# Kernel optimization log

Measured on AMD Instinct MI355X. Metric: run time of the kernel, lower is better.

The kernel has to match this reference:

```python
import jax, jax.numpy as jnp
import numpy as np

H = 8
D = 64
EPS = 1e-5
TEMP = 1.0


def _ln(x, w, b):
    m = jnp.mean(x, axis=-1, keepdims=True)
    v = jnp.var(x, axis=-1, keepdims=True)
    return (x - m) * jax.lax.rsqrt(v + EPS) * w + b


def setup_inputs() -> dict:
    key = jax.random.key(0)
    ks = jax.random.split(key, 8)
    B, T, C = 4, 1024, 512
    x = jax.random.normal(ks[0], (B, T, C), dtype=jnp.float32)
    pair = jax.random.normal(ks[1], (B, T, T, H), dtype=jnp.float32)
    mask = jax.random.randint(ks[2], (B, T, T), 0, 2).astype(bool)
    s = 0.02
    return {
        "x": x,
        "pair": pair,
        "mask": mask,
        "norm_w": jnp.ones((C,), jnp.float32),
        "norm_b": jnp.zeros((C,), jnp.float32),
        "qkv_w": jax.random.normal(ks[3], (3 * C, C), jnp.float32) * s,
        "qkv_b": jnp.zeros((3 * C,), jnp.float32),
        "qln_w": jnp.ones((C,), jnp.float32),
        "qln_b": jnp.zeros((C,), jnp.float32),
        "kln_w": jnp.ones((C,), jnp.float32),
        "kln_b": jnp.zeros((C,), jnp.float32),
        "proj_w": jax.random.normal(ks[4], (C, C), jnp.float32) * s,
        "proj_b": jnp.zeros((C,), jnp.float32),
    }


def reference(x, pair, mask, norm_w, norm_b, qkv_w, qkv_b, qln_w, qln_b,
              kln_w, kln_b, proj_w, proj_b):
    B, T, C = x.shape
    # pre-norm
    xn = _ln(x, norm_w, norm_b)
    qkv = xn @ qkv_w.T + qkv_b  # [B,T,3C]
    q, k, v = jnp.split(qkv, 3, axis=-1)
    q = _ln(q, qln_w, qln_b)
    k = _ln(k, kln_w, kln_b)
    # [B,T,C] -> [B,H,T,D]
    to_heads = lambda t: t.reshape(B, T, H, D).transpose(0, 2, 1, 3)
    q, k, v = to_heads(q), to_heads(k), to_heads(v)
    scale = (D ** -0.5) / TEMP
    sim = jnp.einsum("bhid,bhjd->bhij", q, k) * scale
    sim = sim + pair.transpose(0, 3, 1, 2)  # additive pair bias [B,H,T,T]
    neg = jnp.finfo(sim.dtype).min
    sim = jnp.where(mask[:, None, :, :], sim, sim + neg)
    attn = jax.nn.softmax(sim, axis=-1)
    out = jnp.einsum("bhij,bhjd->bhid", attn, v)
    out = out.transpose(0, 2, 1, 3).reshape(B, T, C)
    return out @ proj_w.T + proj_b
```

## Files before the change

### kernel.cpp

```cpp
#include <hip/hip_runtime.h>
#include <math.h>

#define B_  4
#define T_  1024
#define C_  512
#define H_  8
#define D_  64
#define N3_ 1536
#define BT_ 4096

constexpr float kEps = 1e-5f;
constexpr float kNeg = -3.4028234663852886e38f;
constexpr float kMaskNeg = -1e38f;
constexpr float kShift = 12.0f;

typedef __attribute__((ext_vector_type(8))) short bf16x8;
typedef __attribute__((ext_vector_type(4))) float f32x4;

__device__ __forceinline__ short f2bf(float f) {
  union { float f; unsigned u; } v; v.f = f;
  unsigned r = v.u + 0x7FFFu + ((v.u >> 16) & 1u);
  return (short)(r >> 16);
}
__device__ __forceinline__ float bf2f(unsigned short b) {
  union { unsigned u; float f; } v;
  v.u = ((unsigned)b) << 16;
  return v.f;
}

__device__ __forceinline__ void gld16(const void* g, void* l) {
  __builtin_amdgcn_global_load_lds(
      (const __attribute__((address_space(1))) unsigned int*)g,
      (__attribute__((address_space(3))) unsigned int*)l, 16, 0, 0);
}

__global__ __launch_bounds__(64) void mask_detect_kernel(
    const unsigned int* __restrict__ m, int* __restrict__ flag) {
  int lane = threadIdx.x;
  int any_big = 0;
#pragma unroll
  for (int p = 0; p < 16; ++p) {
    unsigned int v = m[lane + p * 64];
    any_big |= (v > 1u);
  }
  unsigned long long b = __ballot(any_big);
  if (lane == 0) flag[0] = (b != 0ull) ? 1 : 0;
}

__global__ __launch_bounds__(256) void mask_convert_kernel(
    const void* __restrict__ mraw, const int* __restrict__ flag,
    uchar4* __restrict__ out) {
  int idx = blockIdx.x * 256 + threadIdx.x;
  uchar4 v;
  if (flag[0]) {
    v = ((const uchar4*)mraw)[idx];
    v.x = v.x ? 1 : 0; v.y = v.y ? 1 : 0; v.z = v.z ? 1 : 0; v.w = v.w ? 1 : 0;
  } else {
    int4 w = ((const int4*)mraw)[idx];
    v = make_uchar4(w.x != 0, w.y != 0, w.z != 0, w.w != 0);
  }
  out[idx] = v;
}

__global__ __launch_bounds__(256) void pair_prep_kernel(
    const float* __restrict__ pair, const void* __restrict__ mraw,
    short* __restrict__ biast) {
  __shared__ short P[8][1024 + 8];
  unsigned wv = ((const unsigned*)mraw)[threadIdx.x];
  int is_u8 = __syncthreads_or(wv > 1u);
  int bi = blockIdx.x;
  int b = bi >> 10, i = bi & 1023;
  int tid = threadIdx.x;
  const float* src = pair + (size_t)bi * (T_ * H_);
#pragma unroll
  for (int p = 0; p < 8; ++p) {
    int c = tid + p * 256;
    int j = c >> 1, hh = (c & 1) * 4;
    float4 v = *(const float4*)&src[c * 4];
    P[hh + 0][j] = f2bf(v.x);
    P[hh + 1][j] = f2bf(v.y);
    P[hh + 2][j] = f2bf(v.z);
    P[hh + 3][j] = f2bf(v.w);
  }
  bool mk[4];
  if (is_u8) {
    uchar4 mv = ((const uchar4*)mraw)[bi * 256 + tid];
    mk[0] = mv.x; mk[1] = mv.y; mk[2] = mv.z; mk[3] = mv.w;
  } else {
    int4 mv = ((const int4*)mraw)[bi * 256 + tid];
    mk[0] = mv.x != 0; mk[1] = mv.y != 0; mk[2] = mv.z != 0; mk[3] = mv.w != 0;
  }
  __syncthreads();
  const short negb = f2bf(kMaskNeg);
  int j = tid * 4;
#pragma unroll
  for (int h = 0; h < 8; ++h) {
    short4 o;
    o.x = mk[0] ? P[h][j + 0] : negb;
    o.y = mk[1] ? P[h][j + 1] : negb;
    o.z = mk[2] ? P[h][j + 2] : negb;
    o.w = mk[3] ? P[h][j + 3] : negb;
    *(short4*)&biast[((size_t)(b * 8 + h) * T_ + i) * T_ + j] = o;
  }
}

__global__ __launch_bounds__(256) void wcvt2_kernel(
    const float* __restrict__ a, short* __restrict__ oa,
    const float* __restrict__ b, short* __restrict__ ob, int nblk_a) {
  int bid = blockIdx.x;
  const float* src; short* dst; int idx;
  if (bid < nblk_a) { src = a; dst = oa; idx = bid * 256 + threadIdx.x; }
  else             { src = b; dst = ob; idx = (bid - nblk_a) * 256 + threadIdx.x; }
  int i = idx * 4;
  float4 v = *(const float4*)&src[i];
  short4 o;
  o.x = f2bf(v.x); o.y = f2bf(v.y); o.z = f2bf(v.z); o.w = f2bf(v.w);
  *(short4*)&dst[i] = o;
}

__global__ __launch_bounds__(128) void ln_x_kernel(
    const float* __restrict__ x, const float* __restrict__ w,
    const float* __restrict__ b, short* __restrict__ xn) {
  int row = blockIdx.x;
  int tid = threadIdx.x;
  const float* xr = x + (size_t)row * C_;
  float4 v = *(const float4*)&xr[tid * 4];
  float s  = v.x + v.y + v.z + v.w;
  float ss = v.x * v.x + v.y * v.y + v.z * v.z + v.w * v.w;
#pragma unroll
  for (int o = 32; o > 0; o >>= 1) {
    s  += __shfl_down(s, o);
    ss += __shfl_down(ss, o);
  }
  __shared__ float sh[4];
  int wid = tid >> 6, lane = tid & 63;
  if (lane == 0) { sh[wid] = s; sh[2 + wid] = ss; }
  __syncthreads();
  float m   = (sh[0] + sh[1]) * (1.0f / C_);
  float var = (sh[2] + sh[3]) * (1.0f / C_) - m * m;
  float inv = rsqrtf(var + kEps);
  float4 wv = *(const float4*)&w[tid * 4];
  float4 bv = *(const float4*)&b[tid * 4];
  short4 o4;
  o4.x = f2bf((v.x - m) * inv * wv.x + bv.x);
  o4.y = f2bf((v.y - m) * inv * wv.y + bv.y);
  o4.z = f2bf((v.z - m) * inv * wv.z + bv.z);
  o4.w = f2bf((v.w - m) * inv * wv.w + bv.w);
  *(short4*)&xn[(size_t)row * C_ + tid * 4] = o4;
}

__global__ __launch_bounds__(256) void gemm_bf16_kernel(
    const short* __restrict__ A, const short* __restrict__ W,
    const float* __restrict__ bias, float* __restrict__ Cmat,
    int M, int N, int K) {
  __shared__ short As[128 * 64];
  __shared__ short Bs[64 * 64];
  int tid = threadIdx.x;
  int lane = tid & 63, wave = tid >> 6;
  int wm = wave >> 1, wn = wave & 1;
  int col = lane & 15, quad = lane >> 4;
  int m0 = blockIdx.y * 128, n0 = blockIdx.x * 64;
  int wbase = tid & ~63;

  f32x4 acc[4][2];
#pragma unroll
  for (int mi = 0; mi < 4; ++mi)
#pragma unroll
    for (int ni = 0; ni < 2; ++ni) acc[mi][ni] = {0.f, 0.f, 0.f, 0.f};

  for (int k0 = 0; k0 < K; k0 += 64) {
    __syncthreads();
#pragma unroll
    for (int p = 0; p < 4; ++p) {
      int c = tid + p * 256;
      int row = c >> 3, kc = (c & 7) * 8;
      gld16(&A[(size_t)(m0 + row) * K + k0 + kc],
            &As[(wbase + p * 256) * 8]);
    }
#pragma unroll
    for (int p = 0; p < 2; ++p) {
      int c = tid + p * 256;
      int row = c >> 3, kc = (c & 7) * 8;
      gld16(&W[(size_t)(n0 + row) * K + k0 + kc],
            &Bs[(wbase + p * 256) * 8]);
    }
    __syncthreads();
#pragma unroll
    for (int s = 0; s < 2; ++s) {
      bf16x8 af[4], bf[2];
#pragma unroll
      for (int mi = 0; mi < 4; ++mi)
        af[mi] = *(const bf16x8*)&As[(64 * wm + 16 * mi + col) * 64 + s * 32 + quad * 8];
#pragma unroll
      for (int ni = 0; ni < 2; ++ni)
        bf[ni] = *(const bf16x8*)&Bs[(32 * wn + 16 * ni + col) * 64 + s * 32 + quad * 8];
#pragma unroll
      for (int mi = 0; mi < 4; ++mi)
#pragma unroll
        for (int ni = 0; ni < 2; ++ni)
          acc[mi][ni] = __builtin_amdgcn_mfma_f32_16x16x32_bf16(
              af[mi], bf[ni], acc[mi][ni], 0, 0, 0);
    }
  }
#pragma unroll
  for (int ni = 0; ni < 2; ++ni) {
    int n = n0 + 32 * wn + 16 * ni + col;
    float bv = bias[n];
#pragma unroll
    for (int mi = 0; mi < 4; ++mi) {
#pragma unroll
      for (int r = 0; r < 4; ++r) {
        int m = m0 + 64 * wm + 16 * mi + quad * 4 + r;
        Cmat[(size_t)m * N + n] = acc[mi][ni][r] + bv;
      }
    }
  }
}

__global__ __launch_bounds__(128) void qkv_ln_split_kernel(
    const float* __restrict__ qkv,
    const float* __restrict__ qw, const float* __restrict__ qb,
    const float* __restrict__ kw, const float* __restrict__ kb,
    short* __restrict__ qh, short* __restrict__ kh, short* __restrict__ vh) {
  int row = blockIdx.x;
  int b = row >> 10, t = row & 1023;
  int tid = threadIdx.x;
  const float* base = qkv + (size_t)row * N3_;
  int c4 = tid * 4;
  float4 qv = *(const float4*)&base[c4];
  float4 kv = *(const float4*)&base[C_ + c4];
  float4 vv = *(const float4*)&base[2 * C_ + c4];
  float sq  = qv.x + qv.y + qv.z + qv.w;
  float sqq = qv.x * qv.x + qv.y * qv.y + qv.z * qv.z + qv.w * qv.w;
  float sk  = kv.x + kv.y + kv.z + kv.w;
  float skk = kv.x * kv.x + kv.y * kv.y + kv.z * kv.z + kv.w * kv.w;
#pragma unroll
  for (int o = 32; o > 0; o >>= 1) {
    sq  += __shfl_down(sq, o);
    sqq += __shfl_down(sqq, o);
    sk  += __shfl_down(sk, o);
    skk += __shfl_down(skk, o);
  }
  __shared__ float sh[8];
  int wid = tid >> 6, lane = tid & 63;
  if (lane == 0) { sh[wid] = sq; sh[2 + wid] = sqq; sh[4 + wid] = sk; sh[6 + wid] = skk; }
  __syncthreads();
  float qm   = (sh[0] + sh[1]) * (1.0f / C_);
  float qvar = (sh[2] + sh[3]) * (1.0f / C_) - qm * qm;
  float km   = (sh[4] + sh[5]) * (1.0f / C_);
  float kvar = (sh[6] + sh[7]) * (1.0f / C_) - km * km;
  float qi = rsqrtf(qvar + kEps);
  float ki = rsqrtf(kvar + kEps);
  float4 qwv = *(const float4*)&qw[c4];
  float4 qbv = *(const float4*)&qb[c4];
  float4 kwv = *(const float4*)&kw[c4];
  float4 kbv = *(const float4*)&kb[c4];
  int h = tid >> 4;
  int d = (tid & 15) * 4;
  size_t dst = ((size_t)(b * H_ + h) * T_ + t) * D_ + d;
  short4 qo, ko, vo;
  qo.x = f2bf(((qv.x - qm) * qi * qwv.x + qbv.x) * 0.125f);
  qo.y = f2bf(((qv.y - qm) * qi * qwv.y + qbv.y) * 0.125f);
  qo.z = f2bf(((qv.z - qm) * qi * qwv.z + qbv.z) * 0.125f);
  qo.w = f2bf(((qv.w - qm) * qi * qwv.w + qbv.w) * 0.125f);
  ko.x = f2bf((kv.x - km) * ki * kwv.x + kbv.x);
  ko.y = f2bf((kv.y - km) * ki * kwv.y + kbv.y);
  ko.z = f2bf((kv.z - km) * ki * kwv.z + kbv.z);
  ko.w = f2bf((kv.w - km) * ki * kwv.w + kbv.w);
  vo.x = f2bf(vv.x); vo.y = f2bf(vv.y); vo.z = f2bf(vv.z); vo.w = f2bf(vv.w);
  *(short4*)&qh[dst] = qo;
  *(short4*)&kh[dst] = ko;
  *(short4*)&vh[dst] = vo;
}

__global__ __launch_bounds__(256) void attn_split_kernel(
    const short* __restrict__ qh, const short* __restrict__ kh,
    const short* __restrict__ vh, const short* __restrict__ biast,
    float* __restrict__ Opart, float* __restrict__ lpart) {
  __shared__ short Ks[64 * 72];
  __shared__ short Vt[64 * 72];
  __shared__ short Ps[64 * 72];
  int tid = threadIdx.x;
  int lane = tid & 63, w = tid >> 6;
  int col = lane & 15, quad = lane >> 4;
  int bh = blockIdx.y;
  int half = blockIdx.z;
  int i0 = blockIdx.x * 64;
  const short* Qg = qh + (size_t)bh * T_ * D_;
  const short* Kg = kh + (size_t)bh * T_ * D_;
  const short* Vg = vh + (size_t)bh * T_ * D_;
  const unsigned short* Bpu =
      (const unsigned short*)(biast + (size_t)bh * T_ * T_);

  bf16x8 qf[2];
#pragma unroll
  for (int s = 0; s < 2; ++s)
    qf[s] = *(const bf16x8*)&Qg[(size_t)(i0 + 16 * w + col) * D_ + s * 32 + quad * 8];

  float lsum[4];
  f32x4 oacc[4];
#pragma unroll
  for (int r = 0; r < 4; ++r) lsum[r] = 0.f;
#pragma unroll
  for (int dt = 0; dt < 4; ++dt) oacc[dt] = {0.f, 0.f, 0.f, 0.f};

  int jbase = half * (T_ / 2);
  for (int jj = 0; jj < T_ / 2; jj += 64) {
    int j0 = jbase + jj;
    __syncthreads();
#pragma unroll
    for (int p = 0; p < 2; ++p) {
      int c = tid + p * 256;
      int row = c >> 3, dc = (c & 7) * 8;
      *(int4*)&Ks[row * 72 + dc] =
          *(const int4*)&Kg[(size_t)(j0 + row) * D_ + dc];
    }
    {
      int j = tid & 63, d0 = (tid >> 6) * 16;
#pragma unroll
      for (int p = 0; p < 2; ++p) {
        short tmp[8];
        *(int4*)tmp = *(const int4*)&Vg[(size_t)(j0 + j) * D_ + d0 + p * 8];
#pragma unroll
        for (int q = 0; q < 8; ++q) Vt[(d0 + p * 8 + q) * 72 + j] = tmp[q];
      }
    }
    __syncthreads();

    unsigned short bsv[4][4];
#pragma unroll
    for (int r = 0; r < 4; ++r) {
      int gi = i0 + 16 * w + quad * 4 + r;
#pragma unroll
      for (int jt = 0; jt < 4; ++jt)
        bsv[r][jt] = Bpu[(size_t)gi * T_ + j0 + 16 * jt + col];
    }

    f32x4 sacc[4];
#pragma unroll
    for (int jt = 0; jt < 4; ++jt) sacc[jt] = {0.f, 0.f, 0.f, 0.f};
#pragma unroll
    for (int s = 0; s < 2; ++s) {
#pragma unroll
      for (int jt = 0; jt < 4; ++jt) {
        bf16x8 kf = *(const bf16x8*)&Ks[(16 * jt + col) * 72 + s * 32 + quad * 8];
        sacc[jt] = __builtin_amdgcn_mfma_f32_16x16x32_bf16(qf[s], kf, sacc[jt], 0, 0, 0);
      }
    }

#pragma unroll
    for (int r = 0; r < 4; ++r) {
      int li = 16 * w + quad * 4 + r;
#pragma unroll
      for (int jt = 0; jt < 4; ++jt) {
        float s = sacc[jt][r] + bf2f(bsv[r][jt]);
        float p = __expf(fminf(s - kShift, 60.0f));
        lsum[r] += p;
        Ps[li * 72 + 16 * jt + col] = f2bf(p);
      }
    }
    __syncthreads();

#pragma unroll
    for (int s = 0; s < 2; ++s) {
      bf16x8 pf = *(const bf16x8*)&Ps[(16 * w + col) * 72 + s * 32 + quad * 8];
#pragma unroll
      for (int dt = 0; dt < 4; ++dt) {
        bf16x8 vf = *(const bf16x8*)&Vt[(16 * dt + col) * 72 + s * 32 + quad * 8];
        oacc[dt] = __builtin_amdgcn_mfma_f32_16x16x32_bf16(pf, vf, oacc[dt], 0, 0, 0);
      }
    }
  }

#pragma unroll
  for (int r = 0; r < 4; ++r) {
    float l = lsum[r];
#pragma unroll
    for (int o = 1; o < 16; o <<= 1) l += __shfl_xor(l, o);
    int gi = i0 + 16 * w + quad * 4 + r;
    size_t orow = (size_t)half * 32768 + (size_t)bh * T_ + gi;
    if (col == 0) lpart[orow] = l;
#pragma unroll
    for (int dt = 0; dt < 4; ++dt)
      Opart[orow * 64 + 16 * dt + col] = oacc[dt][r];
  }
}

__global__ __launch_bounds__(256) void attn_merge_kernel(
    const float* __restrict__ Opart, const float* __restrict__ lpart,
    short* __restrict__ ao) {
  int g = blockIdx.x * 256 + threadIdx.x;
  int row = g >> 4, d4 = (g & 15) * 4;
  float4 o0 = *(const float4*)&Opart[(size_t)row * 64 + d4];
  float4 o1 = *(const float4*)&Opart[((size_t)32768 + row) * 64 + d4];
  float inv = 1.0f / (lpart[row] + lpart[32768 + row]);
  int bh = row >> 10, gi = row & 1023;
  int b = bh >> 3, h = bh & 7;
  short4 o;
  o.x = f2bf((o0.x + o1.x) * inv);
  o.y = f2bf((o0.y + o1.y) * inv);
  o.z = f2bf((o0.z + o1.z) * inv);
  o.w = f2bf((o0.w + o1.w) * inv);
  *(short4*)&ao[((size_t)(b * T_ + gi)) * C_ + h * D_ + d4] = o;
}

__global__ __launch_bounds__(256) void attn_kernel(
    const short* __restrict__ qh, const short* __restrict__ kh,
    const short* __restrict__ vh, const float* __restrict__ pair,
    const unsigned char* __restrict__ mask, short* __restrict__ ao) {
  __shared__ short Ks[64 * 72];
  __shared__ short Vt[64 * 72];
  __shared__ short Ps[64 * 72];
  int tid = threadIdx.x;
  int lane = tid & 63, w = tid >> 6;
  int col = lane & 15, quad = lane >> 4;
  int bh = blockIdx.y;
  int b = bh >> 3, h = bh & 7;
  int i0 = blockIdx.x * 64;
  const short* Qg = qh + (size_t)bh * T_ * D_;
  const short* Kg = kh + (size_t)bh * T_ * D_;
  const short* Vg = vh + (size_t)bh * T_ * D_;

  bf16x8 qf[2];
#pragma unroll
  for (int s = 0; s < 2; ++s)
    qf[s] = *(const bf16x8*)&Qg[(size_t)(i0 + 16 * w + col) * D_ + s * 32 + quad * 8];

  float mrun[4], lrun[4];
  f32x4 oacc[4];
#pragma unroll
  for (int r = 0; r < 4; ++r) { mrun[r] = -INFINITY; lrun[r] = 0.f; }
#pragma unroll
  for (int dt = 0; dt < 4; ++dt) oacc[dt] = {0.f, 0.f, 0.f, 0.f};

  for (int j0 = 0; j0 < T_; j0 += 64) {
    __syncthreads();
#pragma unroll
    for (int p = 0; p < 2; ++p) {
      int c = tid + p * 256;
      int row = c >> 3, dc = (c & 7) * 8;
      *(int4*)&Ks[row * 72 + dc] =
          *(const int4*)&Kg[(size_t)(j0 + row) * D_ + dc];
    }
    {
      int j = tid & 63, d0 = (tid >> 6) * 16;
#pragma unroll
      for (int p = 0; p < 2; ++p) {
        short tmp[8];
        *(int4*)tmp = *(const int4*)&Vg[(size_t)(j0 + j) * D_ + d0 + p * 8];
#pragma unroll
        for (int q = 0; q < 8; ++q) Vt[(d0 + p * 8 + q) * 72 + j] = tmp[q];
      }
    }
    __syncthreads();

    f32x4 sacc[4];
#pragma unroll
    for (int jt = 0; jt < 4; ++jt) sacc[jt] = {0.f, 0.f, 0.f, 0.f};
#pragma unroll
    for (int s = 0; s < 2; ++s) {
#pragma unroll
      for (int jt = 0; jt < 4; ++jt) {
        bf16x8 kf = *(const bf16x8*)&Ks[(16 * jt + col) * 72 + s * 32 + quad * 8];
        sacc[jt] = __builtin_amdgcn_mfma_f32_16x16x32_bf16(qf[s], kf, sacc[jt], 0, 0, 0);
      }
    }

#pragma unroll
    for (int r = 0; r < 4; ++r) {
      int gi = i0 + 16 * w + quad * 4 + r;
      const float* prow = pair + (size_t)(b * T_ + gi) * (T_ * H_) + h;
      const unsigned char* mrow = mask + (size_t)(b * T_ + gi) * T_;
      float sv[4];
      float rm = -INFINITY;
#pragma unroll
      for (int jt = 0; jt < 4; ++jt) {
        int j = j0 + 16 * jt + col;
        float s = sacc[jt][r] + prow[(size_t)j * H_];
        if (!mrow[j]) s += kNeg;
        sv[jt] = s;
        rm = fmaxf(rm, s);
      }
#pragma unroll
      for (int o = 8; o > 0; o >>= 1) rm = fmaxf(rm, __shfl_xor(rm, o));
      float mnew  = fmaxf(mrun[r], rm);
      float alpha = __expf(mrun[r] - mnew);
      float psum = 0.f;
#pragma unroll
      for (int jt = 0; jt < 4; ++jt) {
        float p = __expf(sv[jt] - mnew);
        psum += p;
        Ps[(16 * w + quad * 4 + r) * 72 + 16 * jt + col] = f2bf(p);
      }
#pragma unroll
      for (int o = 8; o > 0; o >>= 1) psum += __shfl_xor(psum, o);
      lrun[r] = lrun[r] * alpha + psum;
      mrun[r] = mnew;
#pragma unroll
      for (int dt = 0; dt < 4; ++dt) oacc[dt][r] *= alpha;
    }
    __syncthreads();

#pragma unroll
    for (int s = 0; s < 2; ++s) {
      bf16x8 pf = *(const bf16x8*)&Ps[(16 * w + col) * 72 + s * 32 + quad * 8];
#pragma unroll
      for (int dt = 0; dt < 4; ++dt) {
        bf16x8 vf = *(const bf16x8*)&Vt[(16 * dt + col) * 72 + s * 32 + quad * 8];
        oacc[dt] = __builtin_amdgcn_mfma_f32_16x16x32_bf16(pf, vf, oacc[dt], 0, 0, 0);
      }
    }
  }

#pragma unroll
  for (int r = 0; r < 4; ++r) {
    int gi = i0 + 16 * w + quad * 4 + r;
    float inv = 1.0f / lrun[r];
    size_t base = (size_t)(b * T_ + gi) * C_ + h * D_;
#pragma unroll
    for (int dt = 0; dt < 4; ++dt)
      ao[base + 16 * dt + col] = f2bf(oacc[dt][r] * inv);
  }
}

extern "C" void kernel_launch(void* const* d_in, const int* in_sizes, int n_in,
                              void* d_out, int out_size, void* d_ws, size_t ws_size,
                              hipStream_t stream) {
  const float* x      = (const float*)d_in[0];
  const float* pair   = (const float*)d_in[1];
  const void*  maskraw = d_in[2];
  const float* norm_w = (const float*)d_in[3];
  const float* norm_b = (const float*)d_in[4];
  const float* qkv_w  = (const float*)d_in[5];
  const float* qkv_b  = (const float*)d_in[6];
  const float* qln_w  = (const float*)d_in[7];
  const float* qln_b  = (const float*)d_in[8];
  const float* kln_w  = (const float*)d_in[9];
  const float* kln_b  = (const float*)d_in[10];
  const float* proj_w = (const float*)d_in[11];
  const float* proj_b = (const float*)d_in[12];
  float* out = (float*)d_out;

  short* xn = (short*)d_out;
  short* qh = (short*)d_out + (size_t)BT_ * C_;

  const size_t MB = 1024 * 1024;

  if (ws_size >= 96 * MB) {
    char* base = (char*)d_ws;
    short* biast = (short*)base;
    float* qkv   = (float*)base;
    float* Opart = (float*)(base + 64 * MB);
    float* lpart = (float*)(base + 80 * MB);
    short* ao    = (short*)(base + 81 * MB);
    short* kh    = (short*)(base + 85 * MB);
    short* vh    = (short*)(base + 89 * MB);
    short* wq    = (short*)(base + 93 * MB);
    short* wp    = (short*)(base + 94 * MB + 512 * 1024);

    wcvt2_kernel<<<(N3_ * C_ + C_ * C_) / 1024, 256, 0, stream>>>(
        qkv_w, wq, proj_w, wp, (N3_ * C_) / 1024);
    ln_x_kernel<<<BT_, 128, 0, stream>>>(x, norm_w, norm_b, xn);
    gemm_bf16_kernel<<<dim3(N3_ / 64, BT_ / 128), 256, 0, stream>>>(
        xn, wq, qkv_b, qkv, BT_, N3_, C_);
    qkv_ln_split_kernel<<<BT_, 128, 0, stream>>>(
        qkv, qln_w, qln_b, kln_w, kln_b, qh, kh, vh);
    pair_prep_kernel<<<B_ * T_, 256, 0, stream>>>(pair, maskraw, biast);
    attn_split_kernel<<<dim3(T_ / 64, B_ * H_, 2), 256, 0, stream>>>(
        qh, kh, vh, biast, Opart, lpart);
    attn_merge_kernel<<<2048, 256, 0, stream>>>(Opart, lpart, ao);
    gemm_bf16_kernel<<<dim3(C_ / 64, BT_ / 128), 256, 0, stream>>>(
        ao, wp, proj_b, out, BT_, C_, C_);
  } else {
    float* qkv = (float*)d_ws;
    short* ao  = (short*)d_ws;
    short* sw  = (short*)d_ws;
    short* wq  = sw + (size_t)12 * 1024 * 1024;
    short* wp  = wq + (size_t)N3_ * C_;
    short* kh  = sw + (size_t)13 * 1024 * 1024;
    short* vh  = sw + (size_t)15 * 1024 * 1024;
    unsigned char* maskc = (unsigned char*)d_ws + (size_t)34 * MB;
    int* flag = (int*)((unsigned char*)d_ws + (size_t)38 * MB);

    mask_detect_kernel<<<1, 64, 0, stream>>>((const unsigned int*)maskraw, flag);
    mask_convert_kernel<<<(B_ * T_ * T_) / 1024, 256, 0, stream>>>(
        maskraw, flag, (uchar4*)maskc);
    wcvt2_kernel<<<(N3_ * C_ + C_ * C_) / 1024, 256, 0, stream>>>(
        qkv_w, wq, proj_w, wp, (N3_ * C_) / 1024);
    ln_x_kernel<<<BT_, 128, 0, stream>>>(x, norm_w, norm_b, xn);
    gemm_bf16_kernel<<<dim3(N3_ / 64, BT_ / 128), 256, 0, stream>>>(
        xn, wq, qkv_b, qkv, BT_, N3_, C_);
    qkv_ln_split_kernel<<<BT_, 128, 0, stream>>>(
        qkv, qln_w, qln_b, kln_w, kln_b, qh, kh, vh);
    attn_kernel<<<dim3(T_ / 64, B_ * H_), 256, 0, stream>>>(
        qh, kh, vh, pair, maskc, ao);
    gemm_bf16_kernel<<<dim3(C_ / 64, BT_ / 128), 256, 0, stream>>>(
        ao, wp, proj_b, out, BT_, C_, C_);
  }
}
```

Measured before the change: 308.1 us.

## Fuse pair bias and mask gather into attention, drop bias precompute kernel

Removes the separate pass that converted pair bias to a masked bf16 [B,H,T,T] tensor. The attention kernel now reads the fp32 pair tensor and the raw mask directly, strided by head, and folds them into an exp2-based softmax with log2e prescaling. The attention tile grows to 128 query rows with 512 threads, and a redundant barrier after the P write is dropped. Workspace is also shrunk by aliasing K onto the output buffer. This saves the 64MB intermediate write and read, but each lane now does scattered 4-byte gathers at a 32-byte stride. Across heads this relies on cache reuse, and if that reuse fails it could raise effective DRAM traffic.

```diff
diff --git a/kernel.cpp b/kernel.cpp
--- a/kernel.cpp
+++ b/kernel.cpp
@@ -11,8 +11,9 @@
 
 constexpr float kEps = 1e-5f;
 constexpr float kNeg = -3.4028234663852886e38f;
-constexpr float kMaskNeg = -1e38f;
-constexpr float kShift = 12.0f;
+constexpr float kMaskNeg = -1.4e38f;
+constexpr float kLog2e = 1.44269504088896f;
+constexpr float kShift2 = 17.312340490667562f;
 
 typedef __attribute__((ext_vector_type(8))) short bf16x8;
 typedef __attribute__((ext_vector_type(4))) float f32x4;
@@ -60,48 +61,6 @@
     v = make_uchar4(w.x != 0, w.y != 0, w.z != 0, w.w != 0);
   }
   out[idx] = v;
-}
-
-__global__ __launch_bounds__(256) void pair_prep_kernel(
-    const float* __restrict__ pair, const void* __restrict__ mraw,
-    short* __restrict__ biast) {
-  __shared__ short P[8][1024 + 8];
-  unsigned wv = ((const unsigned*)mraw)[threadIdx.x];
-  int is_u8 = __syncthreads_or(wv > 1u);
-  int bi = blockIdx.x;
-  int b = bi >> 10, i = bi & 1023;
-  int tid = threadIdx.x;
-  const float* src = pair + (size_t)bi * (T_ * H_);
-#pragma unroll
-  for (int p = 0; p < 8; ++p) {
-    int c = tid + p * 256;
-    int j = c >> 1, hh = (c & 1) * 4;
-    float4 v = *(const float4*)&src[c * 4];
-    P[hh + 0][j] = f2bf(v.x);
-    P[hh + 1][j] = f2bf(v.y);
-    P[hh + 2][j] = f2bf(v.z);
-    P[hh + 3][j] = f2bf(v.w);
-  }
-  bool mk[4];
-  if (is_u8) {
-    uchar4 mv = ((const uchar4*)mraw)[bi * 256 + tid];
-    mk[0] = mv.x; mk[1] = mv.y; mk[2] = mv.z; mk[3] = mv.w;
-  } else {
-    int4 mv = ((const int4*)mraw)[bi * 256 + tid];
-    mk[0] = mv.x != 0; mk[1] = mv.y != 0; mk[2] = mv.z != 0; mk[3] = mv.w != 0;
-  }
-  __syncthreads();
-  const short negb = f2bf(kMaskNeg);
-  int j = tid * 4;
-#pragma unroll
-  for (int h = 0; h < 8; ++h) {
-    short4 o;
-    o.x = mk[0] ? P[h][j + 0] : negb;
-    o.y = mk[1] ? P[h][j + 1] : negb;
-    o.z = mk[2] ? P[h][j + 2] : negb;
-    o.w = mk[3] ? P[h][j + 3] : negb;
-    *(short4*)&biast[((size_t)(b * 8 + h) * T_ + i) * T_ + j] = o;
-  }
 }
 
 __global__ __launch_bounds__(256) void wcvt2_kernel(
@@ -174,32 +133,30 @@
     for (int p = 0; p < 4; ++p) {
       int c = tid + p * 256;
       int row = c >> 3, kc = (c & 7) * 8;
-      gld16(&A[(size_t)(m0 + row) * K + k0 + kc],
-            &As[(wbase + p * 256) * 8]);
+      gld16(&A[(size_t)(m0 + row) * K + k0 + kc], &As[(wbase + p * 256) * 8]);
     }
 #pragma unroll
     for (int p = 0; p < 2; ++p) {
       int c = tid + p * 256;
       int row = c >> 3, kc = (c & 7) * 8;
-      gld16(&W[(size_t)(n0 + row) * K + k0 + kc],
-            &Bs[(wbase + p * 256) * 8]);
+      gld16(&W[(size_t)(n0 + row) * K + k0 + kc], &Bs[(wbase + p * 256) * 8]);
     }
     __syncthreads();
 #pragma unroll
     for (int s = 0; s < 2; ++s) {
-      bf16x8 af[4], bf[2];
+      bf16x8 af[4], bfv[2];
 #pragma unroll
       for (int mi = 0; mi < 4; ++mi)
         af[mi] = *(const bf16x8*)&As[(64 * wm + 16 * mi + col) * 64 + s * 32 + quad * 8];
 #pragma unroll
       for (int ni = 0; ni < 2; ++ni)
-        bf[ni] = *(const bf16x8*)&Bs[(32 * wn + 16 * ni + col) * 64 + s * 32 + quad * 8];
+        bfv[ni] = *(const bf16x8*)&Bs[(32 * wn + 16 * ni + col) * 64 + s * 32 + quad * 8];
 #pragma unroll
       for (int mi = 0; mi < 4; ++mi)
 #pragma unroll
         for (int ni = 0; ni < 2; ++ni)
           acc[mi][ni] = __builtin_amdgcn_mfma_f32_16x16x32_bf16(
-              af[mi], bf[ni], acc[mi][ni], 0, 0, 0);
+              af[mi], bfv[ni], acc[mi][ni], 0, 0, 0);
     }
   }
 #pragma unroll
@@ -273,24 +230,30 @@
   *(short4*)&vh[dst] = vo;
 }
 
-__global__ __launch_bounds__(256) void attn_split_kernel(
+__global__ __launch_bounds__(512, 4) void attn_split_kernel(
     const short* __restrict__ qh, const short* __restrict__ kh,
-    const short* __restrict__ vh, const short* __restrict__ biast,
+    const short* __restrict__ vh, const float* __restrict__ pair,
+    const void* __restrict__ mraw,
     float* __restrict__ Opart, float* __restrict__ lpart) {
   __shared__ short Ks[64 * 72];
   __shared__ short Vt[64 * 72];
-  __shared__ short Ps[64 * 72];
+  __shared__ short Ps[128 * 72];
   int tid = threadIdx.x;
   int lane = tid & 63, w = tid >> 6;
   int col = lane & 15, quad = lane >> 4;
   int bh = blockIdx.y;
+  int b = bh >> 3, h = bh & 7;
   int half = blockIdx.z;
-  int i0 = blockIdx.x * 64;
+  int i0 = blockIdx.x * 128;
+
+  unsigned wv = ((const unsigned*)mraw)[tid];
+  int is_u8 = __syncthreads_or(wv > 1u);
+  int mshift = is_u8 ? 0 : 2;
+  const unsigned char* mbase = (const unsigned char*)mraw;
+
   const short* Qg = qh + (size_t)bh * T_ * D_;
   const short* Kg = kh + (size_t)bh * T_ * D_;
   const short* Vg = vh + (size_t)bh * T_ * D_;
-  const unsigned short* Bpu =
-      (const unsigned short*)(biast + (size_t)bh * T_ * T_);
 
   bf16x8 qf[2];
 #pragma unroll
@@ -308,32 +271,33 @@
   for (int jj = 0; jj < T_ / 2; jj += 64) {
     int j0 = jbase + jj;
     __syncthreads();
-#pragma unroll
-    for (int p = 0; p < 2; ++p) {
-      int c = tid + p * 256;
-      int row = c >> 3, dc = (c & 7) * 8;
+    {
+      int row = tid >> 3, dc = (tid & 7) * 8;
       *(int4*)&Ks[row * 72 + dc] =
           *(const int4*)&Kg[(size_t)(j0 + row) * D_ + dc];
     }
     {
-      int j = tid & 63, d0 = (tid >> 6) * 16;
-#pragma unroll
-      for (int p = 0; p < 2; ++p) {
-        short tmp[8];
-        *(int4*)tmp = *(const int4*)&Vg[(size_t)(j0 + j) * D_ + d0 + p * 8];
-#pragma unroll
-        for (int q = 0; q < 8; ++q) Vt[(d0 + p * 8 + q) * 72 + j] = tmp[q];
-      }
-    }
-    __syncthreads();
-
-    unsigned short bsv[4][4];
+      int j = tid & 63, d0 = (tid >> 6) * 8;
+      short tmp[8];
+      *(int4*)tmp = *(const int4*)&Vg[(size_t)(j0 + j) * D_ + d0];
+#pragma unroll
+      for (int q = 0; q < 8; ++q) Vt[(d0 + q) * 72 + j] = tmp[q];
+    }
+    __syncthreads();
+
+    float bias_eff[4][4];
 #pragma unroll
     for (int r = 0; r < 4; ++r) {
       int gi = i0 + 16 * w + quad * 4 + r;
-#pragma unroll
-      for (int jt = 0; jt < 4; ++jt)
-        bsv[r][jt] = Bpu[(size_t)gi * T_ + j0 + 16 * jt + col];
+      const float* prow = pair + ((size_t)(b * T_ + gi) * T_) * H_ + h;
+      const unsigned char* mrow = mbase + (((size_t)(b * T_ + gi) * T_) << mshift);
+#pragma unroll
+      for (int jt = 0; jt < 4; ++jt) {
+        int j = j0 + 16 * jt + col;
+        float pv = prow[(size_t)j * H_];
+        unsigned char mv = mrow[(size_t)j << mshift];
+        bias_eff[r][jt] = mv ? pv * kLog2e : kMaskNeg;
+      }
     }
 
     f32x4 sacc[4];
@@ -353,13 +317,12 @@
       int li = 16 * w + quad * 4 + r;
 #pragma unroll
       for (int jt = 0; jt < 4; ++jt) {
-        float s = sacc[jt][r] + bf2f(bsv[r][jt]);
-        float p = __expf(fminf(s - kShift, 60.0f));
+        float sv = fmaf(sacc[jt][r], kLog2e, bias_eff[r][jt]);
+        float p = exp2f(fminf(sv - kShift2, 86.5f));
         lsum[r] += p;
         Ps[li * 72 + 16 * jt + col] = f2bf(p);
       }
     }
-    __syncthreads();
 
 #pragma unroll
     for (int s = 0; s < 2; ++s) {
@@ -541,22 +504,20 @@
   const float* proj_b = (const float*)d_in[12];
   float* out = (float*)d_out;
 
-  short* xn = (short*)d_out;
-  short* qh = (short*)d_out + (size_t)BT_ * C_;
-
   const size_t MB = 1024 * 1024;
 
-  if (ws_size >= 96 * MB) {
+  if (ws_size >= 52 * MB) {
     char* base = (char*)d_ws;
-    short* biast = (short*)base;
     float* qkv   = (float*)base;
-    float* Opart = (float*)(base + 64 * MB);
-    float* lpart = (float*)(base + 80 * MB);
-    short* ao    = (short*)(base + 81 * MB);
-    short* kh    = (short*)(base + 85 * MB);
-    short* vh    = (short*)(base + 89 * MB);
-    short* wq    = (short*)(base + 93 * MB);
-    short* wp    = (short*)(base + 94 * MB + 512 * 1024);
+    float* Opart = (float*)(base + 24 * MB);
+    float* lpart = (float*)(base + 40 * MB);
+    short* ao    = (short*)(base + 41 * MB);
+    short* vh    = (short*)(base + 45 * MB);
+    short* wq    = (short*)(base + 49 * MB);
+    short* wp    = (short*)(base + 50 * MB + 512 * 1024);
+    short* xn = (short*)d_out;
+    short* kh = (short*)d_out;
+    short* qh = (short*)d_out + (size_t)BT_ * C_;
 
     wcvt2_kernel<<<(N3_ * C_ + C_ * C_) / 1024, 256, 0, stream>>>(
         qkv_w, wq, proj_w, wp, (N3_ * C_) / 1024);
@@ -565,13 +526,14 @@
         xn, wq, qkv_b, qkv, BT_, N3_, C_);
     qkv_ln_split_kernel<<<BT_, 128, 0, stream>>>(
         qkv, qln_w, qln_b, kln_w, kln_b, qh, kh, vh);
-    pair_prep_kernel<<<B_ * T_, 256, 0, stream>>>(pair, maskraw, biast);
-    attn_split_kernel<<<dim3(T_ / 64, B_ * H_, 2), 256, 0, stream>>>(
-        qh, kh, vh, biast, Opart, lpart);
+    attn_split_kernel<<<dim3(T_ / 128, B_ * H_, 2), 512, 0, stream>>>(
+        qh, kh, vh, pair, maskraw, Opart, lpart);
     attn_merge_kernel<<<2048, 256, 0, stream>>>(Opart, lpart, ao);
     gemm_bf16_kernel<<<dim3(C_ / 64, BT_ / 128), 256, 0, stream>>>(
         ao, wp, proj_b, out, BT_, C_, C_);
   } else {
+    short* xn = (short*)d_out;
+    short* qh = (short*)d_out + (size_t)BT_ * C_;
     float* qkv = (float*)d_ws;
     short* ao  = (short*)d_ws;
     short* sw  = (short*)d_ws;
```

Result: slower. 353.8 us (+14.8%).

## Double attention query tile to 128 rows, use exp2 with prescaled bias

Applied to the files above, without the earlier changes.

The attention kernel now runs 512 threads per block and covers 128 query rows, so each staged K/V tile is reused by twice as many waves and per-thread load work halves. The pair bias is prescaled by log2(e) during prep, so softmax can use exp2f with a fused multiply-add instead of __expf. The barrier between writing P to shared memory and reading it back is removed, which relies on each wave reading only its own P rows. The larger block raises register and LDS pressure per block, and the epilogue code that is not shown must already handle the new row mapping.

```diff
diff --git a/kernel.cpp b/kernel.cpp
--- a/kernel.cpp
+++ b/kernel.cpp
@@ -11,8 +11,9 @@
 
 constexpr float kEps = 1e-5f;
 constexpr float kNeg = -3.4028234663852886e38f;
-constexpr float kMaskNeg = -1e38f;
-constexpr float kShift = 12.0f;
+constexpr float kMaskNeg = -1.4e38f;
+constexpr float kLog2e = 1.44269504088896f;
+constexpr float kShift2 = 17.312340490667562f;
 
 typedef __attribute__((ext_vector_type(8))) short bf16x8;
 typedef __attribute__((ext_vector_type(4))) float f32x4;
@@ -77,10 +78,10 @@
     int c = tid + p * 256;
     int j = c >> 1, hh = (c & 1) * 4;
     float4 v = *(const float4*)&src[c * 4];
-    P[hh + 0][j] = f2bf(v.x);
-    P[hh + 1][j] = f2bf(v.y);
-    P[hh + 2][j] = f2bf(v.z);
-    P[hh + 3][j] = f2bf(v.w);
+    P[hh + 0][j] = f2bf(v.x * kLog2e);
+    P[hh + 1][j] = f2bf(v.y * kLog2e);
+    P[hh + 2][j] = f2bf(v.z * kLog2e);
+    P[hh + 3][j] = f2bf(v.w * kLog2e);
   }
   bool mk[4];
   if (is_u8) {
@@ -174,32 +175,30 @@
     for (int p = 0; p < 4; ++p) {
       int c = tid + p * 256;
       int row = c >> 3, kc = (c & 7) * 8;
-      gld16(&A[(size_t)(m0 + row) * K + k0 + kc],
-            &As[(wbase + p * 256) * 8]);
+      gld16(&A[(size_t)(m0 + row) * K + k0 + kc], &As[(wbase + p * 256) * 8]);
     }
 #pragma unroll
     for (int p = 0; p < 2; ++p) {
       int c = tid + p * 256;
       int row = c >> 3, kc = (c & 7) * 8;
-      gld16(&W[(size_t)(n0 + row) * K + k0 + kc],
-            &Bs[(wbase + p * 256) * 8]);
+      gld16(&W[(size_t)(n0 + row) * K + k0 + kc], &Bs[(wbase + p * 256) * 8]);
     }
     __syncthreads();
 #pragma unroll
     for (int s = 0; s < 2; ++s) {
-      bf16x8 af[4], bf[2];
+      bf16x8 af[4], bfv[2];
 #pragma unroll
       for (int mi = 0; mi < 4; ++mi)
         af[mi] = *(const bf16x8*)&As[(64 * wm + 16 * mi + col) * 64 + s * 32 + quad * 8];
 #pragma unroll
       for (int ni = 0; ni < 2; ++ni)
-        bf[ni] = *(const bf16x8*)&Bs[(32 * wn + 16 * ni + col) * 64 + s * 32 + quad * 8];
+        bfv[ni] = *(const bf16x8*)&Bs[(32 * wn + 16 * ni + col) * 64 + s * 32 + quad * 8];
 #pragma unroll
       for (int mi = 0; mi < 4; ++mi)
 #pragma unroll
         for (int ni = 0; ni < 2; ++ni)
           acc[mi][ni] = __builtin_amdgcn_mfma_f32_16x16x32_bf16(
-              af[mi], bf[ni], acc[mi][ni], 0, 0, 0);
+              af[mi], bfv[ni], acc[mi][ni], 0, 0, 0);
     }
   }
 #pragma unroll
@@ -273,19 +272,19 @@
   *(short4*)&vh[dst] = vo;
 }
 
-__global__ __launch_bounds__(256) void attn_split_kernel(
+__global__ __launch_bounds__(512, 4) void attn_split_kernel(
     const short* __restrict__ qh, const short* __restrict__ kh,
     const short* __restrict__ vh, const short* __restrict__ biast,
     float* __restrict__ Opart, float* __restrict__ lpart) {
   __shared__ short Ks[64 * 72];
   __shared__ short Vt[64 * 72];
-  __shared__ short Ps[64 * 72];
+  __shared__ short Ps[128 * 72];
   int tid = threadIdx.x;
   int lane = tid & 63, w = tid >> 6;
   int col = lane & 15, quad = lane >> 4;
   int bh = blockIdx.y;
   int half = blockIdx.z;
-  int i0 = blockIdx.x * 64;
+  int i0 = blockIdx.x * 128;
   const short* Qg = qh + (size_t)bh * T_ * D_;
   const short* Kg = kh + (size_t)bh * T_ * D_;
   const short* Vg = vh + (size_t)bh * T_ * D_;
@@ -308,22 +307,17 @@
   for (int jj = 0; jj < T_ / 2; jj += 64) {
     int j0 = jbase + jj;
     __syncthreads();
-#pragma unroll
-    for (int p = 0; p < 2; ++p) {
-      int c = tid + p * 256;
-      int row = c >> 3, dc = (c & 7) * 8;
+    {
+      int row = tid >> 3, dc = (tid & 7) * 8;
       *(int4*)&Ks[row * 72 + dc] =
           *(const int4*)&Kg[(size_t)(j0 + row) * D_ + dc];
     }
     {
-      int j = tid & 63, d0 = (tid >> 6) * 16;
-#pragma unroll
-      for (int p = 0; p < 2; ++p) {
-        short tmp[8];
-        *(int4*)tmp = *(const int4*)&Vg[(size_t)(j0 + j) * D_ + d0 + p * 8];
-#pragma unroll
-        for (int q = 0; q < 8; ++q) Vt[(d0 + p * 8 + q) * 72 + j] = tmp[q];
-      }
+      int j = tid & 63, d0 = (tid >> 6) * 8;
+      short tmp[8];
+      *(int4*)tmp = *(const int4*)&Vg[(size_t)(j0 + j) * D_ + d0];
+#pragma unroll
+      for (int q = 0; q < 8; ++q) Vt[(d0 + q) * 72 + j] = tmp[q];
     }
     __syncthreads();
 
@@ -353,13 +347,12 @@
       int li = 16 * w + quad * 4 + r;
 #pragma unroll
       for (int jt = 0; jt < 4; ++jt) {
-        float s = sacc[jt][r] + bf2f(bsv[r][jt]);
-        float p = __expf(fminf(s - kShift, 60.0f));
+        float sv = fmaf(sacc[jt][r], kLog2e, bf2f(bsv[r][jt]));
+        float p = exp2f(fminf(sv - kShift2, 86.5f));
         lsum[r] += p;
         Ps[li * 72 + 16 * jt + col] = f2bf(p);
       }
     }
-    __syncthreads();
 
 #pragma unroll
     for (int s = 0; s < 2; ++s) {
@@ -566,7 +559,7 @@
     qkv_ln_split_kernel<<<BT_, 128, 0, stream>>>(
         qkv, qln_w, qln_b, kln_w, kln_b, qh, kh, vh);
     pair_prep_kernel<<<B_ * T_, 256, 0, stream>>>(pair, maskraw, biast);
-    attn_split_kernel<<<dim3(T_ / 64, B_ * H_, 2), 256, 0, stream>>>(
+    attn_split_kernel<<<dim3(T_ / 128, B_ * H_, 2), 512, 0, stream>>>(
         qh, kh, vh, biast, Opart, lpart);
     attn_merge_kernel<<<2048, 256, 0, stream>>>(Opart, lpart, ao);
     gemm_bf16_kernel<<<dim3(C_ / 64, BT_ / 128), 256, 0, stream>>>(
```

Result: slower. 314.6 us (+2.1%).
